# Performance work log

Hardware: AMD Instinct MI355X
Metric: run time of the kernel (lower is better)

## Reference

```python
import jax, jax.numpy as jnp
import numpy as np

MAX_SIZE = 650   # hard-coded node count in the original module
HIDDEN = 512     # hidden_dim
BATCH = 512      # batch_size (conv4 out channels)
IN_DIM = 512
N_EDGES = 150000


def _segment_softmax(e, dst, n):
    # torch_geometric.utils.softmax over destination-node segments
    m = jax.ops.segment_max(e, dst, num_segments=n)
    ex = jnp.exp(e - m[dst])
    s = jax.ops.segment_sum(ex, dst, num_segments=n)
    return ex / (s[dst] + 1e-16)


def _gat_conv(x, src, dst, W, a_src, a_dst, b, n, neg_slope=0.2):
    # PyG GATConv, heads=1, edge_dim=None (edge_attr ignored)
    h = x @ W                            # [n, out]
    al_s = h @ a_src                     # [n] per-node source attention logit
    al_d = h @ a_dst                     # [n] per-node dest attention logit
    e = jax.nn.leaky_relu(al_s[src] + al_d[dst], neg_slope)   # [E]
    alpha = _segment_softmax(e, dst, n)                        # [E]
    out = jax.ops.segment_sum(alpha[:, None] * h[src], dst, num_segments=n)
    return out + b


def setup_inputs() -> dict:
    key = jax.random.key(0)
    ks = jax.random.split(key, 12)
    inp = {
        "x_s": jax.random.normal(ks[0], (400, IN_DIM), jnp.float32),
        "x_t": jax.random.normal(ks[1], (250, IN_DIM), jnp.float32),
        "edge_index": jax.random.randint(ks[2], (2, N_EDGES), 0, MAX_SIZE, dtype=jnp.int32),
        "distances": jax.random.uniform(ks[3], (N_EDGES,), jnp.float32),
        "batch": jnp.zeros((MAX_SIZE,), jnp.int32),
        "W1": jax.random.normal(ks[4], (IN_DIM, HIDDEN), jnp.float32) / np.sqrt(IN_DIM).astype(np.float32),
        "a_src1": jax.random.normal(ks[5], (HIDDEN,), jnp.float32) * 0.1,
        "a_dst1": jax.random.normal(ks[6], (HIDDEN,), jnp.float32) * 0.1,
        "b1": jnp.zeros((HIDDEN,), jnp.float32),
        "W4": jax.random.normal(ks[7], (HIDDEN, BATCH), jnp.float32) / np.sqrt(HIDDEN).astype(np.float32),
        "a_src4": jax.random.normal(ks[8], (BATCH,), jnp.float32) * 0.1,
        "a_dst4": jax.random.normal(ks[9], (BATCH,), jnp.float32) * 0.1,
        "b4": jnp.zeros((BATCH,), jnp.float32),
        "fc_w": jax.random.normal(ks[10], (1, MAX_SIZE), jnp.float32) / np.sqrt(MAX_SIZE).astype(np.float32),
        "fc_b": jnp.zeros((1,), jnp.float32),
    }
    return inp


def reference(x_s, x_t, edge_index, distances, batch,
              W1, a_src1, a_dst1, b1, W4, a_src4, a_dst4, b4, fc_w, fc_b):
    # distances (edge_attr) and batch are unpacked but unused, as in the
    # original (GATConv with edge_dim=None ignores edge_attr).
    x = jnp.concatenate([x_s, x_t], axis=0)
    pad_n = max(MAX_SIZE - x.shape[0], 0)
    x = jnp.pad(x, ((0, pad_n), (0, 0)))            # [650, IN_DIM]
    # add_self_loops=True (PyG GATConv default)
    loop = jnp.arange(MAX_SIZE, dtype=edge_index.dtype)
    src = jnp.concatenate([edge_index[0], loop])
    dst = jnp.concatenate([edge_index[1], loop])
    x = _gat_conv(x, src, dst, W1, a_src1, a_dst1, b1, MAX_SIZE)
    x = jax.nn.relu(x)
    x = _gat_conv(x, src, dst, W4, a_src4, a_dst4, b4, MAX_SIZE)
    x = jax.nn.leaky_relu(x, 0.01)                  # [650, BATCH]
    x = x.reshape(BATCH, MAX_SIZE)                  # torch .view semantics (no transpose)
    x = x @ fc_w.T + fc_b                           # [BATCH, 1]
    x = x.squeeze()[None, :]                        # [1, BATCH]
    return jax.nn.sigmoid(x)
```

## Files before the change

### kernel.cpp

```cpp
#include <hip/hip_runtime.h>
#include <math.h>

#define N_NODES 650
#define DIM     512
#define E_RAW   150000
#define E_TOT   150650
#define WK      672
#define ZG      8
#define ZA      6

__global__ __launch_bounds__(256)
void gemm4(const float* __restrict__ A, const float* __restrict__ Axt,
           const float* __restrict__ B, float* __restrict__ P,
           int M, int lda, int ldb, int kc, int a_mode) {
    __shared__ float Ast[16][68];
    __shared__ float Bs[16][64];
    int t = threadIdx.x;
    int tx4 = (t & 15) * 4, ty4 = (t >> 4) * 4;
    int row0 = blockIdx.y * 64, col0 = blockIdx.x * 64;
    int kbase = blockIdx.z * kc;
    int ar = t >> 2, ak = (t & 3) * 4;
    int bk = t >> 4, bn = (t & 15) * 4;
    float acc[4][4] = {};

    for (int kb = kbase; kb < kbase + kc; kb += 16) {
        {
            int gr = row0 + ar;
            float4 v = make_float4(0.f, 0.f, 0.f, 0.f);
            if (gr < M) {
                const float* rowp;
                if (a_mode == 1)
                    rowp = (gr < 400) ? (A + (size_t)gr * lda) : (Axt + (size_t)(gr - 400) * lda);
                else
                    rowp = A + (size_t)gr * lda;
                v = *(const float4*)(rowp + kb + ak);
            }
            Ast[ak + 0][ar] = v.x; Ast[ak + 1][ar] = v.y;
            Ast[ak + 2][ar] = v.z; Ast[ak + 3][ar] = v.w;
        }
        *(float4*)&Bs[bk][bn] = *(const float4*)&B[(size_t)(kb + bk) * ldb + col0 + bn];
        __syncthreads();
        #pragma unroll
        for (int kk = 0; kk < 16; kk++) {
            float4 a = *(const float4*)&Ast[kk][ty4];
            float4 b = *(const float4*)&Bs[kk][tx4];
            acc[0][0] += a.x*b.x; acc[0][1] += a.x*b.y; acc[0][2] += a.x*b.z; acc[0][3] += a.x*b.w;
            acc[1][0] += a.y*b.x; acc[1][1] += a.y*b.y; acc[1][2] += a.y*b.z; acc[1][3] += a.y*b.w;
            acc[2][0] += a.z*b.x; acc[2][1] += a.z*b.y; acc[2][2] += a.z*b.z; acc[2][3] += a.z*b.w;
            acc[3][0] += a.w*b.x; acc[3][1] += a.w*b.y; acc[3][2] += a.w*b.z; acc[3][3] += a.w*b.w;
        }
        __syncthreads();
    }

    float* Cout = P + (size_t)blockIdx.z * (N_NODES * DIM);
    #pragma unroll
    for (int i = 0; i < 4; i++) {
        int gr = row0 + ty4 + i;
        if (gr < M)
            *(float4*)&Cout[(size_t)gr * DIM + col0 + tx4] =
                make_float4(acc[i][0], acc[i][1], acc[i][2], acc[i][3]);
    }
}

__global__ __launch_bounds__(256)
void reduce_logits(const float* __restrict__ P,
                   const float* __restrict__ asrc, const float* __restrict__ adst,
                   float* __restrict__ h, float* __restrict__ als, float* __restrict__ ald) {
    __shared__ float red[8];
    const size_t S = (size_t)N_NODES * DIM;
    int r = blockIdx.x, t = threadIdx.x;
    size_t base = (size_t)r * DIM;
    float v0 = 0.f, v1 = 0.f;
    #pragma unroll
    for (int z = 0; z < ZG; z++) {
        v0 += P[z * S + base + t];
        v1 += P[z * S + base + t + 256];
    }
    h[base + t]       = v0;
    h[base + t + 256] = v1;
    float ps = v0 * asrc[t] + v1 * asrc[t + 256];
    float pd = v0 * adst[t] + v1 * adst[t + 256];
    #pragma unroll
    for (int o = 32; o > 0; o >>= 1) {
        ps += __shfl_down(ps, o);
        pd += __shfl_down(pd, o);
    }
    if ((t & 63) == 0) { red[t >> 6] = ps; red[4 + (t >> 6)] = pd; }
    __syncthreads();
    if (t == 0) als[r] = red[0] + red[1] + red[2] + red[3];
    if (t == 1) ald[r] = red[4] + red[5] + red[6] + red[7];
}

__global__ __launch_bounds__(256)
void build_w(const int* __restrict__ ei, const float* __restrict__ als,
             const float* __restrict__ ald, float* __restrict__ W,
             float* __restrict__ rs) {
    __shared__ float lrs[N_NODES];
    for (int l = threadIdx.x; l < N_NODES; l += 256) lrs[l] = 0.f;
    __syncthreads();
    int stride = gridDim.x * 256;
    for (int i = blockIdx.x * 256 + threadIdx.x; i < E_TOT; i += stride) {
        int s, d;
        if (i < E_RAW) { s = ei[i]; d = ei[E_RAW + i]; }
        else           { s = d = i - E_RAW; }
        float e = als[s] + ald[d];
        e = e > 0.f ? e : 0.2f * e;
        float ex = __expf(e);
        atomicAdd(&W[(size_t)d * WK + s], ex);
        atomicAdd(&lrs[d], ex);
    }
    __syncthreads();
    for (int l = threadIdx.x; l < N_NODES; l += 256)
        if (lrs[l] != 0.f) atomicAdd(&rs[l], lrs[l]);
}

__global__ __launch_bounds__(256)
void aggred(const float* __restrict__ P, const float* __restrict__ rs,
            const float* __restrict__ bias, float slope, float* __restrict__ o) {
    const size_t S = (size_t)N_NODES * DIM;
    int r = blockIdx.x, t = threadIdx.x;
    size_t base = (size_t)r * DIM;
    float v0 = 0.f, v1 = 0.f;
    #pragma unroll
    for (int z = 0; z < ZA; z++) {
        v0 += P[z * S + base + t];
        v1 += P[z * S + base + t + 256];
    }
    float inv = 1.f / (rs[r] + 1e-16f);
    float a = v0 * inv + bias[t];
    float b = v1 * inv + bias[t + 256];
    o[base + t]       = a > 0.f ? a : slope * a;
    o[base + t + 256] = b > 0.f ? b : slope * b;
}

__global__ void final_kernel(const float* __restrict__ o2,
                             const float* __restrict__ fcw,
                             const float* __restrict__ fcb,
                             float* __restrict__ out) {
    int b = blockIdx.x * 4 + (threadIdx.x >> 6);
    int lane = threadIdx.x & 63;
    if (b >= 512) return;
    float s = 0.f;
    for (int i = lane; i < N_NODES; i += 64)
        s += o2[b * N_NODES + i] * fcw[i];
    #pragma unroll
    for (int o = 32; o > 0; o >>= 1) s += __shfl_down(s, o);
    if (lane == 0) out[b] = 1.f / (1.f + expf(-(s + fcb[0])));
}

extern "C" void kernel_launch(void* const* d_in, const int* in_sizes, int n_in,
                              void* d_out, int out_size, void* d_ws, size_t ws_size,
                              hipStream_t stream) {
    const float* x_s   = (const float*)d_in[0];
    const float* x_t   = (const float*)d_in[1];
    const int*   ei    = (const int*)d_in[2];
    const float* W1    = (const float*)d_in[5];
    const float* asrc1 = (const float*)d_in[6];
    const float* adst1 = (const float*)d_in[7];
    const float* b1    = (const float*)d_in[8];
    const float* W4    = (const float*)d_in[9];
    const float* asrc4 = (const float*)d_in[10];
    const float* adst4 = (const float*)d_in[11];
    const float* b4    = (const float*)d_in[12];
    const float* fcw   = (const float*)d_in[13];
    const float* fcb   = (const float*)d_in[14];
    float* out = (float*)d_out;

    const size_t S = (size_t)N_NODES * DIM;
    float* ws   = (float*)d_ws;
    float* als1 = ws;
    float* ald1 = als1 + N_NODES;
    float* als2 = ald1 + N_NODES;
    float* ald2 = als2 + N_NODES;
    float* P    = ald2 + N_NODES;
    float* o1   = P + (size_t)ZG * S;
    float* o2   = o1 + S;
    float* h    = o2 + S;
    float* W1d  = h + (size_t)WK * DIM;
    float* W2d  = W1d + (size_t)N_NODES * WK;
    float* rs1  = W2d + (size_t)N_NODES * WK;
    float* rs2  = rs1 + N_NODES;

    float* zbeg = h + (size_t)N_NODES * DIM;
    size_t zbytes = (size_t)((WK - N_NODES) * DIM
                           + 2 * N_NODES * WK
                           + 2 * N_NODES) * sizeof(float);
    hipMemsetAsync(zbeg, 0, zbytes, stream);

    dim3 gG(DIM / 64, (N_NODES + 63) / 64, ZG);
    dim3 gA(DIM / 64, (N_NODES + 63) / 64, ZA);

    gemm4<<<gG, 256, 0, stream>>>(x_s, x_t, W1, P, N_NODES, DIM, DIM, 64, 1);
    reduce_logits<<<N_NODES, 256, 0, stream>>>(P, asrc1, adst1, h, als1, ald1);
    build_w<<<128, 256, 0, stream>>>(ei, als1, ald1, W1d, rs1);
    gemm4<<<gA, 256, 0, stream>>>(W1d, nullptr, h, P, N_NODES, WK, DIM, 112, 0);
    aggred<<<N_NODES, 256, 0, stream>>>(P, rs1, b1, 0.0f, o1);

    gemm4<<<gG, 256, 0, stream>>>(o1, nullptr, W4, P, N_NODES, DIM, DIM, 64, 0);
    reduce_logits<<<N_NODES, 256, 0, stream>>>(P, asrc4, adst4, h, als2, ald2);
    build_w<<<128, 256, 0, stream>>>(ei, als2, ald2, W2d, rs2);
    gemm4<<<gA, 256, 0, stream>>>(W2d, nullptr, h, P, N_NODES, WK, DIM, 112, 0);
    aggred<<<N_NODES, 256, 0, stream>>>(P, rs2, b4, 0.01f, o2);

    final_kernel<<<128, 256, 0, stream>>>(o2, fcw, fcb, out);
}
```

Before: 194.7 us.

## Fuse all GAT stages into one cooperative persistent kernel with grid syncs

Replaces the sequence of eleven kernel launches plus a memset with a single cooperative kernel that loops over virtual tiles and rows and separates the stages with grid-wide barriers. Zeroing is done inside the kernel. The aim is to remove per-launch overhead and the idle gaps between the small kernels. The cost is a grid capped at 512 blocks, so the GEMM phases get fewer concurrent blocks than their original tile counts (704 and 528 tiles), and each grid sync adds barrier latency. A non-cooperative fallback path is kept.

```diff
diff --git a/kernel.cpp b/kernel.cpp
--- a/kernel.cpp
+++ b/kernel.cpp
@@ -1,5 +1,8 @@
 #include <hip/hip_runtime.h>
+#include <hip/hip_cooperative_groups.h>
 #include <math.h>
+
+namespace cg = cooperative_groups;
 
 #define N_NODES 650
 #define DIM     512
@@ -8,98 +11,108 @@
 #define WK      672
 #define ZG      8
 #define ZA      6
-
-__global__ __launch_bounds__(256)
-void gemm4(const float* __restrict__ A, const float* __restrict__ Axt,
-           const float* __restrict__ B, float* __restrict__ P,
-           int M, int lda, int ldb, int kc, int a_mode) {
-    __shared__ float Ast[16][68];
-    __shared__ float Bs[16][64];
+#define TILES_X 8
+#define TILES_Y 11
+
+__device__ __forceinline__
+void gemm_phase(const float* __restrict__ A, const float* __restrict__ Axt,
+                const float* __restrict__ B, float* __restrict__ P,
+                int lda, int ldb, int kc, int nvirt, int a_mode, int G,
+                float (* __restrict__ Ast)[68], float (* __restrict__ Bs)[64]) {
     int t = threadIdx.x;
     int tx4 = (t & 15) * 4, ty4 = (t >> 4) * 4;
-    int row0 = blockIdx.y * 64, col0 = blockIdx.x * 64;
-    int kbase = blockIdx.z * kc;
     int ar = t >> 2, ak = (t & 3) * 4;
     int bk = t >> 4, bn = (t & 15) * 4;
-    float acc[4][4] = {};
-
-    for (int kb = kbase; kb < kbase + kc; kb += 16) {
-        {
-            int gr = row0 + ar;
-            float4 v = make_float4(0.f, 0.f, 0.f, 0.f);
-            if (gr < M) {
-                const float* rowp;
-                if (a_mode == 1)
-                    rowp = (gr < 400) ? (A + (size_t)gr * lda) : (Axt + (size_t)(gr - 400) * lda);
-                else
-                    rowp = A + (size_t)gr * lda;
-                v = *(const float4*)(rowp + kb + ak);
+
+    for (int vb = blockIdx.x; vb < nvirt; vb += G) {
+        int bx  = vb & (TILES_X - 1);
+        int rem = vb >> 3;
+        int by  = rem % TILES_Y;
+        int bz  = rem / TILES_Y;
+        int row0 = by * 64, col0 = bx * 64, kbase = bz * kc;
+        float acc[4][4] = {};
+
+        for (int kb = kbase; kb < kbase + kc; kb += 16) {
+            {
+                int gr = row0 + ar;
+                float4 v = make_float4(0.f, 0.f, 0.f, 0.f);
+                if (gr < N_NODES) {
+                    const float* rowp;
+                    if (a_mode == 1)
+                        rowp = (gr < 400) ? (A + (size_t)gr * lda) : (Axt + (size_t)(gr - 400) * lda);
+                    else
+                        rowp = A + (size_t)gr * lda;
+                    v = *(const float4*)(rowp + kb + ak);
+                }
+                Ast[ak + 0][ar] = v.x; Ast[ak + 1][ar] = v.y;
+                Ast[ak + 2][ar] = v.z; Ast[ak + 3][ar] = v.w;
             }
-            Ast[ak + 0][ar] = v.x; Ast[ak + 1][ar] = v.y;
-            Ast[ak + 2][ar] = v.z; Ast[ak + 3][ar] = v.w;
-        }
-        *(float4*)&Bs[bk][bn] = *(const float4*)&B[(size_t)(kb + bk) * ldb + col0 + bn];
+            *(float4*)&Bs[bk][bn] = *(const float4*)&B[(size_t)(kb + bk) * ldb + col0 + bn];
+            __syncthreads();
+            #pragma unroll
+            for (int kk = 0; kk < 16; kk++) {
+                float4 a = *(const float4*)&Ast[kk][ty4];
+                float4 b = *(const float4*)&Bs[kk][tx4];
+                acc[0][0] += a.x*b.x; acc[0][1] += a.x*b.y; acc[0][2] += a.x*b.z; acc[0][3] += a.x*b.w;
+                acc[1][0] += a.y*b.x; acc[1][1] += a.y*b.y; acc[1][2] += a.y*b.z; acc[1][3] += a.y*b.w;
+                acc[2][0] += a.z*b.x; acc[2][1] += a.z*b.y; acc[2][2] += a.z*b.z; acc[2][3] += a.z*b.w;
+                acc[3][0] += a.w*b.x; acc[3][1] += a.w*b.y; acc[3][2] += a.w*b.z; acc[3][3] += a.w*b.w;
+            }
+            __syncthreads();
+        }
+
+        float* Cout = P + (size_t)bz * (N_NODES * DIM);
+        #pragma unroll
+        for (int i = 0; i < 4; i++) {
+            int gr = row0 + ty4 + i;
+            if (gr < N_NODES)
+                *(float4*)&Cout[(size_t)gr * DIM + col0 + tx4] =
+                    make_float4(acc[i][0], acc[i][1], acc[i][2], acc[i][3]);
+        }
+    }
+}
+
+__device__ __forceinline__
+void reduce_phase(const float* __restrict__ P,
+                  const float* __restrict__ asrc, const float* __restrict__ adst,
+                  float* __restrict__ h, float* __restrict__ als, float* __restrict__ ald,
+                  int G, float* __restrict__ red) {
+    const size_t S = (size_t)N_NODES * DIM;
+    int t = threadIdx.x;
+    for (int r = blockIdx.x; r < N_NODES; r += G) {
+        size_t base = (size_t)r * DIM;
+        float v0 = 0.f, v1 = 0.f;
+        #pragma unroll
+        for (int z = 0; z < ZG; z++) {
+            v0 += P[z * S + base + t];
+            v1 += P[z * S + base + t + 256];
+        }
+        h[base + t]       = v0;
+        h[base + t + 256] = v1;
+        float ps = v0 * asrc[t] + v1 * asrc[t + 256];
+        float pd = v0 * adst[t] + v1 * adst[t + 256];
+        #pragma unroll
+        for (int o = 32; o > 0; o >>= 1) {
+            ps += __shfl_down(ps, o);
+            pd += __shfl_down(pd, o);
+        }
+        if ((t & 63) == 0) { red[t >> 6] = ps; red[4 + (t >> 6)] = pd; }
         __syncthreads();
-        #pragma unroll
-        for (int kk = 0; kk < 16; kk++) {
-            float4 a = *(const float4*)&Ast[kk][ty4];
-            float4 b = *(const float4*)&Bs[kk][tx4];
-            acc[0][0] += a.x*b.x; acc[0][1] += a.x*b.y; acc[0][2] += a.x*b.z; acc[0][3] += a.x*b.w;
-            acc[1][0] += a.y*b.x; acc[1][1] += a.y*b.y; acc[1][2] += a.y*b.z; acc[1][3] += a.y*b.w;
-            acc[2][0] += a.z*b.x; acc[2][1] += a.z*b.y; acc[2][2] += a.z*b.z; acc[2][3] += a.z*b.w;
-            acc[3][0] += a.w*b.x; acc[3][1] += a.w*b.y; acc[3][2] += a.w*b.z; acc[3][3] += a.w*b.w;
-        }
+        if (t == 0) als[r] = red[0] + red[1] + red[2] + red[3];
+        if (t == 1) ald[r] = red[4] + red[5] + red[6] + red[7];
         __syncthreads();
     }
-
-    float* Cout = P + (size_t)blockIdx.z * (N_NODES * DIM);
-    #pragma unroll
-    for (int i = 0; i < 4; i++) {
-        int gr = row0 + ty4 + i;
-        if (gr < M)
-            *(float4*)&Cout[(size_t)gr * DIM + col0 + tx4] =
-                make_float4(acc[i][0], acc[i][1], acc[i][2], acc[i][3]);
-    }
-}
-
-__global__ __launch_bounds__(256)
-void reduce_logits(const float* __restrict__ P,
-                   const float* __restrict__ asrc, const float* __restrict__ adst,
-                   float* __restrict__ h, float* __restrict__ als, float* __restrict__ ald) {
-    __shared__ float red[8];
-    const size_t S = (size_t)N_NODES * DIM;
-    int r = blockIdx.x, t = threadIdx.x;
-    size_t base = (size_t)r * DIM;
-    float v0 = 0.f, v1 = 0.f;
-    #pragma unroll
-    for (int z = 0; z < ZG; z++) {
-        v0 += P[z * S + base + t];
-        v1 += P[z * S + base + t + 256];
-    }
-    h[base + t]       = v0;
-    h[base + t + 256] = v1;
-    float ps = v0 * asrc[t] + v1 * asrc[t + 256];
-    float pd = v0 * adst[t] + v1 * adst[t + 256];
-    #pragma unroll
-    for (int o = 32; o > 0; o >>= 1) {
-        ps += __shfl_down(ps, o);
-        pd += __shfl_down(pd, o);
-    }
-    if ((t & 63) == 0) { red[t >> 6] = ps; red[4 + (t >> 6)] = pd; }
+}
+
+__device__ __forceinline__
+void build_phase(const int* __restrict__ ei, const float* __restrict__ als,
+                 const float* __restrict__ ald, float* __restrict__ W,
+                 float* __restrict__ rs, int G, float* __restrict__ lrs) {
+    int t = threadIdx.x;
+    for (int l = t; l < N_NODES; l += 256) lrs[l] = 0.f;
     __syncthreads();
-    if (t == 0) als[r] = red[0] + red[1] + red[2] + red[3];
-    if (t == 1) ald[r] = red[4] + red[5] + red[6] + red[7];
-}
-
-__global__ __launch_bounds__(256)
-void build_w(const int* __restrict__ ei, const float* __restrict__ als,
-             const float* __restrict__ ald, float* __restrict__ W,
-             float* __restrict__ rs) {
-    __shared__ float lrs[N_NODES];
-    for (int l = threadIdx.x; l < N_NODES; l += 256) lrs[l] = 0.f;
-    __syncthreads();
-    int stride = gridDim.x * 256;
-    for (int i = blockIdx.x * 256 + threadIdx.x; i < E_TOT; i += stride) {
+    const int stride = G * 256;
+    for (int i = blockIdx.x * 256 + t; i < E_TOT; i += stride) {
         int s, d;
         if (i < E_RAW) { s = ei[i]; d = ei[E_RAW + i]; }
         else           { s = d = i - E_RAW; }
@@ -110,42 +123,165 @@
         atomicAdd(&lrs[d], ex);
     }
     __syncthreads();
-    for (int l = threadIdx.x; l < N_NODES; l += 256)
+    for (int l = t; l < N_NODES; l += 256)
         if (lrs[l] != 0.f) atomicAdd(&rs[l], lrs[l]);
-}
-
-__global__ __launch_bounds__(256)
-void aggred(const float* __restrict__ P, const float* __restrict__ rs,
-            const float* __restrict__ bias, float slope, float* __restrict__ o) {
+    __syncthreads();
+}
+
+__device__ __forceinline__
+void aggred_phase(const float* __restrict__ P, const float* __restrict__ rs,
+                  const float* __restrict__ bias, float slope, float* __restrict__ o, int G) {
     const size_t S = (size_t)N_NODES * DIM;
-    int r = blockIdx.x, t = threadIdx.x;
-    size_t base = (size_t)r * DIM;
-    float v0 = 0.f, v1 = 0.f;
-    #pragma unroll
-    for (int z = 0; z < ZA; z++) {
-        v0 += P[z * S + base + t];
-        v1 += P[z * S + base + t + 256];
-    }
-    float inv = 1.f / (rs[r] + 1e-16f);
-    float a = v0 * inv + bias[t];
-    float b = v1 * inv + bias[t + 256];
-    o[base + t]       = a > 0.f ? a : slope * a;
-    o[base + t + 256] = b > 0.f ? b : slope * b;
-}
-
-__global__ void final_kernel(const float* __restrict__ o2,
-                             const float* __restrict__ fcw,
-                             const float* __restrict__ fcb,
-                             float* __restrict__ out) {
-    int b = blockIdx.x * 4 + (threadIdx.x >> 6);
-    int lane = threadIdx.x & 63;
-    if (b >= 512) return;
-    float s = 0.f;
-    for (int i = lane; i < N_NODES; i += 64)
-        s += o2[b * N_NODES + i] * fcw[i];
-    #pragma unroll
-    for (int o = 32; o > 0; o >>= 1) s += __shfl_down(s, o);
-    if (lane == 0) out[b] = 1.f / (1.f + expf(-(s + fcb[0])));
+    int t = threadIdx.x;
+    for (int r = blockIdx.x; r < N_NODES; r += G) {
+        size_t base = (size_t)r * DIM;
+        float v0 = 0.f, v1 = 0.f;
+        #pragma unroll
+        for (int z = 0; z < ZA; z++) {
+            v0 += P[z * S + base + t];
+            v1 += P[z * S + base + t + 256];
+        }
+        float inv = 1.f / (rs[r] + 1e-16f);
+        float a = v0 * inv + bias[t];
+        float b = v1 * inv + bias[t + 256];
+        o[base + t]       = a > 0.f ? a : slope * a;
+        o[base + t + 256] = b > 0.f ? b : slope * b;
+    }
+}
+
+__device__ __forceinline__
+void final_phase(const float* __restrict__ o2, const float* __restrict__ fcw,
+                 const float* __restrict__ fcb, float* __restrict__ out,
+                 int G, float* __restrict__ red) {
+    int t = threadIdx.x;
+    for (int b = blockIdx.x; b < 512; b += G) {
+        float s = 0.f;
+        for (int i = t; i < N_NODES; i += 256)
+            s += o2[(size_t)b * N_NODES + i] * fcw[i];
+        #pragma unroll
+        for (int o = 32; o > 0; o >>= 1) s += __shfl_down(s, o);
+        if ((t & 63) == 0) red[t >> 6] = s;
+        __syncthreads();
+        if (t == 0) {
+            float v = red[0] + red[1] + red[2] + red[3] + fcb[0];
+            out[b] = 1.f / (1.f + expf(-v));
+        }
+        __syncthreads();
+    }
+}
+
+__device__ __forceinline__
+void zero_phase(float* __restrict__ zbeg, int nz4, int G) {
+    float4* z4 = (float4*)zbeg;
+    int t = threadIdx.x;
+    for (int i = blockIdx.x * 256 + t; i < nz4; i += G * 256)
+        z4[i] = make_float4(0.f, 0.f, 0.f, 0.f);
+}
+
+__global__ __launch_bounds__(256, 2)
+void gat_fused(const float* __restrict__ x_s, const float* __restrict__ x_t,
+               const int* __restrict__ ei,
+               const float* __restrict__ W1, const float* __restrict__ as1,
+               const float* __restrict__ ad1, const float* __restrict__ b1,
+               const float* __restrict__ W4, const float* __restrict__ as4,
+               const float* __restrict__ ad4, const float* __restrict__ b4,
+               const float* __restrict__ fcw, const float* __restrict__ fcb,
+               float* __restrict__ out, float* __restrict__ ws) {
+    __shared__ float Ast[16][68];
+    __shared__ float Bs[16][64];
+    __shared__ float lrs[N_NODES];
+    __shared__ float red[8];
+
+    const size_t S = (size_t)N_NODES * DIM;
+    float* als1 = ws;
+    float* ald1 = als1 + N_NODES;
+    float* als2 = ald1 + N_NODES;
+    float* ald2 = als2 + N_NODES;
+    float* P    = ald2 + N_NODES;
+    float* o1   = P + (size_t)ZG * S;
+    float* o2   = o1 + S;
+    float* h    = o2 + S;
+    float* W1d  = h + (size_t)WK * DIM;
+    float* W2d  = W1d + (size_t)N_NODES * WK;
+    float* rs1  = W2d + (size_t)N_NODES * WK;
+    float* rs2  = rs1 + N_NODES;
+
+    cg::grid_group grid = cg::this_grid();
+    const int G = gridDim.x;
+
+    {
+        const int nz4 = ((WK - N_NODES) * DIM + 2 * N_NODES * WK + 2 * N_NODES) / 4;
+        zero_phase(h + (size_t)N_NODES * DIM, nz4, G);
+    }
+    gemm_phase(x_s, x_t, W1, P, DIM, DIM, 64, TILES_X * TILES_Y * ZG, 1, G, Ast, Bs);
+    grid.sync();
+
+    reduce_phase(P, as1, ad1, h, als1, ald1, G, red);
+    grid.sync();
+
+    build_phase(ei, als1, ald1, W1d, rs1, G, lrs);
+    grid.sync();
+
+    gemm_phase(W1d, nullptr, h, P, WK, DIM, 112, TILES_X * TILES_Y * ZA, 0, G, Ast, Bs);
+    grid.sync();
+
+    aggred_phase(P, rs1, b1, 0.0f, o1, G);
+    grid.sync();
+
+    gemm_phase(o1, nullptr, W4, P, DIM, DIM, 64, TILES_X * TILES_Y * ZG, 0, G, Ast, Bs);
+    grid.sync();
+
+    reduce_phase(P, as4, ad4, h, als2, ald2, G, red);
+    grid.sync();
+
+    build_phase(ei, als2, ald2, W2d, rs2, G, lrs);
+    grid.sync();
+
+    gemm_phase(W2d, nullptr, h, P, WK, DIM, 112, TILES_X * TILES_Y * ZA, 0, G, Ast, Bs);
+    grid.sync();
+
+    aggred_phase(P, rs2, b4, 0.01f, o2, G);
+    grid.sync();
+
+    final_phase(o2, fcw, fcb, out, G, red);
+}
+
+__global__ __launch_bounds__(256)
+void k_gemm(const float* __restrict__ A, const float* __restrict__ Axt,
+            const float* __restrict__ B, float* __restrict__ P,
+            int lda, int ldb, int kc, int nvirt, int a_mode) {
+    __shared__ float Ast[16][68];
+    __shared__ float Bs[16][64];
+    gemm_phase(A, Axt, B, P, lda, ldb, kc, nvirt, a_mode, gridDim.x, Ast, Bs);
+}
+
+__global__ __launch_bounds__(256)
+void k_reduce(const float* __restrict__ P, const float* __restrict__ asrc,
+              const float* __restrict__ adst, float* __restrict__ h,
+              float* __restrict__ als, float* __restrict__ ald) {
+    __shared__ float red[8];
+    reduce_phase(P, asrc, adst, h, als, ald, gridDim.x, red);
+}
+
+__global__ __launch_bounds__(256)
+void k_build(const int* __restrict__ ei, const float* __restrict__ als,
+             const float* __restrict__ ald, float* __restrict__ W,
+             float* __restrict__ rs) {
+    __shared__ float lrs[N_NODES];
+    build_phase(ei, als, ald, W, rs, gridDim.x, lrs);
+}
+
+__global__ __launch_bounds__(256)
+void k_aggred(const float* __restrict__ P, const float* __restrict__ rs,
+              const float* __restrict__ bias, float slope, float* __restrict__ o) {
+    aggred_phase(P, rs, bias, slope, o, gridDim.x);
+}
+
+__global__ __launch_bounds__(256)
+void k_final(const float* __restrict__ o2, const float* __restrict__ fcw,
+             const float* __restrict__ fcb, float* __restrict__ out) {
+    __shared__ float red[8];
+    final_phase(o2, fcw, fcb, out, gridDim.x, red);
 }
 
 extern "C" void kernel_launch(void* const* d_in, const int* in_sizes, int n_in,
@@ -165,9 +301,9 @@
     const float* fcw   = (const float*)d_in[13];
     const float* fcb   = (const float*)d_in[14];
     float* out = (float*)d_out;
+    float* ws  = (float*)d_ws;
 
     const size_t S = (size_t)N_NODES * DIM;
-    float* ws   = (float*)d_ws;
     float* als1 = ws;
     float* ald1 = als1 + N_NODES;
     float* als2 = ald1 + N_NODES;
@@ -181,26 +317,60 @@
     float* rs1  = W2d + (size_t)N_NODES * WK;
     float* rs2  = rs1 + N_NODES;
 
-    float* zbeg = h + (size_t)N_NODES * DIM;
-    size_t zbytes = (size_t)((WK - N_NODES) * DIM
-                           + 2 * N_NODES * WK
-                           + 2 * N_NODES) * sizeof(float);
-    hipMemsetAsync(zbeg, 0, zbytes, stream);
-
-    dim3 gG(DIM / 64, (N_NODES + 63) / 64, ZG);
-    dim3 gA(DIM / 64, (N_NODES + 63) / 64, ZA);
-
-    gemm4<<<gG, 256, 0, stream>>>(x_s, x_t, W1, P, N_NODES, DIM, DIM, 64, 1);
-    reduce_logits<<<N_NODES, 256, 0, stream>>>(P, asrc1, adst1, h, als1, ald1);
-    build_w<<<128, 256, 0, stream>>>(ei, als1, ald1, W1d, rs1);
-    gemm4<<<gA, 256, 0, stream>>>(W1d, nullptr, h, P, N_NODES, WK, DIM, 112, 0);
-    aggred<<<N_NODES, 256, 0, stream>>>(P, rs1, b1, 0.0f, o1);
-
-    gemm4<<<gG, 256, 0, stream>>>(o1, nullptr, W4, P, N_NODES, DIM, DIM, 64, 0);
-    reduce_logits<<<N_NODES, 256, 0, stream>>>(P, asrc4, adst4, h, als2, ald2);
-    build_w<<<128, 256, 0, stream>>>(ei, als2, ald2, W2d, rs2);
-    gemm4<<<gA, 256, 0, stream>>>(W2d, nullptr, h, P, N_NODES, WK, DIM, 112, 0);
-    aggred<<<N_NODES, 256, 0, stream>>>(P, rs2, b4, 0.01f, o2);
-
-    final_kernel<<<128, 256, 0, stream>>>(o2, fcw, fcb, out);
-}
+    static int coop_blocks = -2;
+    if (coop_blocks == -2) {
+        int maxB = 0;
+        hipError_t e = hipOccupancyMaxActiveBlocksPerMultiprocessor(
+            &maxB, (const void*)gat_fused, 256, 0);
+        if (e == hipSuccess && maxB >= 1) {
+            hipDeviceProp_t prop;
+            int dev = 0;
+            hipGetDevice(&dev);
+            if (hipGetDeviceProperties(&prop, dev) == hipSuccess && prop.multiProcessorCount > 0) {
+                long cap = (long)maxB * prop.multiProcessorCount;
+                coop_blocks = (int)(cap < 512 ? cap : 512);
+            } else {
+                coop_blocks = -1;
+            }
+        } else {
+            coop_blocks = -1;
+        }
+    }
+
+    bool done = false;
+    if (coop_blocks > 0) {
+        void* args[] = {
+            (void*)&x_s, (void*)&x_t, (void*)&ei,
+            (void*)&W1, (void*)&asrc1, (void*)&adst1, (void*)&b1,
+            (void*)&W4, (void*)&asrc4, (void*)&adst4, (void*)&b4,
+            (void*)&fcw, (void*)&fcb, (void*)&out, (void*)&ws
+        };
+        hipError_t e = hipLaunchCooperativeKernel((const void*)gat_fused,
+                                                  dim3(coop_blocks), dim3(256),
+                                                  args, 0, stream);
+        if (e == hipSuccess) done = true;
+        else coop_blocks = -1;
+    }
+
+    if (!done) {
+        float* zbeg = h + (size_t)N_NODES * DIM;
+        size_t zbytes = (size_t)((WK - N_NODES) * DIM
+                               + 2 * N_NODES * WK
+                               + 2 * N_NODES) * sizeof(float);
+        hipMemsetAsync(zbeg, 0, zbytes, stream);
+
+        k_gemm<<<512, 256, 0, stream>>>(x_s, x_t, W1, P, DIM, DIM, 64, TILES_X * TILES_Y * ZG, 1);
+        k_reduce<<<N_NODES, 256, 0, stream>>>(P, asrc1, adst1, h, als1, ald1);
+        k_build<<<128, 256, 0, stream>>>(ei, als1, ald1, W1d, rs1);
+        k_gemm<<<512, 256, 0, stream>>>(W1d, nullptr, h, P, WK, DIM, 112, TILES_X * TILES_Y * ZA, 0);
+        k_aggred<<<N_NODES, 256, 0, stream>>>(P, rs1, b1, 0.0f, o1);
+
+        k_gemm<<<512, 256, 0, stream>>>(o1, nullptr, W4, P, DIM, DIM, 64, TILES_X * TILES_Y * ZG, 0);
+        k_reduce<<<N_NODES, 256, 0, stream>>>(P, asrc4, adst4, h, als2, ald2);
+        k_build<<<128, 256, 0, stream>>>(ei, als2, ald2, W2d, rs2);
+        k_gemm<<<512, 256, 0, stream>>>(W2d, nullptr, h, P, WK, DIM, 112, TILES_X * TILES_Y * ZA, 0);
+        k_aggred<<<N_NODES, 256, 0, stream>>>(P, rs2, b4, 0.01f, o2);
+
+        k_final<<<512, 256, 0, stream>>>(o2, fcw, fcb, out);
+    }
+}
```

Result: slower. 525.0 us (+169.7%).

## Fuse split-K reductions into GEMM epilogues and drop partial-sum buffers

Applied to the files above, without the earlier changes.

Removes split-K from both GEMM stages. Attention logits are computed in the feature GEMM epilogue via shuffles and atomics, and normalization, bias and activation are applied in the aggregation GEMM epilogue. This eliminates the separate reduce kernels and the large partial-sum buffer traffic. In exchange, each GEMM launches far fewer blocks with a much longer K loop, which reduces parallelism across CUs.

```diff
diff --git a/kernel.cpp b/kernel.cpp
--- a/kernel.cpp
+++ b/kernel.cpp
@@ -6,39 +6,36 @@
 #define E_RAW   150000
 #define E_TOT   150650
 #define WK      672
-#define ZG      8
-#define ZA      6
 
 __global__ __launch_bounds__(256)
-void gemm4(const float* __restrict__ A, const float* __restrict__ Axt,
-           const float* __restrict__ B, float* __restrict__ P,
-           int M, int lda, int ldb, int kc, int a_mode) {
+void k_feat(const float* __restrict__ A, const float* __restrict__ Axt,
+            const float* __restrict__ B,
+            const float* __restrict__ asrc, const float* __restrict__ adst,
+            float* __restrict__ h, float* __restrict__ als, float* __restrict__ ald,
+            int a_mode) {
     __shared__ float Ast[16][68];
     __shared__ float Bs[16][64];
     int t = threadIdx.x;
     int tx4 = (t & 15) * 4, ty4 = (t >> 4) * 4;
     int row0 = blockIdx.y * 64, col0 = blockIdx.x * 64;
-    int kbase = blockIdx.z * kc;
     int ar = t >> 2, ak = (t & 3) * 4;
     int bk = t >> 4, bn = (t & 15) * 4;
     float acc[4][4] = {};
 
-    for (int kb = kbase; kb < kbase + kc; kb += 16) {
+    for (int kb = 0; kb < DIM; kb += 16) {
         {
             int gr = row0 + ar;
             float4 v = make_float4(0.f, 0.f, 0.f, 0.f);
-            if (gr < M) {
-                const float* rowp;
-                if (a_mode == 1)
-                    rowp = (gr < 400) ? (A + (size_t)gr * lda) : (Axt + (size_t)(gr - 400) * lda);
-                else
-                    rowp = A + (size_t)gr * lda;
+            if (gr < N_NODES) {
+                const float* rowp = (a_mode == 1)
+                    ? ((gr < 400) ? A + (size_t)gr * DIM : Axt + (size_t)(gr - 400) * DIM)
+                    : A + (size_t)gr * DIM;
                 v = *(const float4*)(rowp + kb + ak);
             }
             Ast[ak + 0][ar] = v.x; Ast[ak + 1][ar] = v.y;
             Ast[ak + 2][ar] = v.z; Ast[ak + 3][ar] = v.w;
         }
-        *(float4*)&Bs[bk][bn] = *(const float4*)&B[(size_t)(kb + bk) * ldb + col0 + bn];
+        *(float4*)&Bs[bk][bn] = *(const float4*)&B[(size_t)(kb + bk) * DIM + col0 + bn];
         __syncthreads();
         #pragma unroll
         for (int kk = 0; kk < 16; kk++) {
@@ -52,54 +49,39 @@
         __syncthreads();
     }
 
-    float* Cout = P + (size_t)blockIdx.z * (N_NODES * DIM);
+    float4 as4 = *(const float4*)&asrc[col0 + tx4];
+    float4 ad4 = *(const float4*)&adst[col0 + tx4];
     #pragma unroll
     for (int i = 0; i < 4; i++) {
         int gr = row0 + ty4 + i;
-        if (gr < M)
-            *(float4*)&Cout[(size_t)gr * DIM + col0 + tx4] =
+        float sa = acc[i][0]*as4.x + acc[i][1]*as4.y + acc[i][2]*as4.z + acc[i][3]*as4.w;
+        float sd = acc[i][0]*ad4.x + acc[i][1]*ad4.y + acc[i][2]*ad4.z + acc[i][3]*ad4.w;
+        #pragma unroll
+        for (int o = 8; o > 0; o >>= 1) {
+            sa += __shfl_down(sa, o, 16);
+            sd += __shfl_down(sd, o, 16);
+        }
+        if (gr < N_NODES) {
+            *(float4*)&h[(size_t)gr * DIM + col0 + tx4] =
                 make_float4(acc[i][0], acc[i][1], acc[i][2], acc[i][3]);
+            if ((t & 15) == 0) {
+                atomicAdd(&als[gr], sa);
+                atomicAdd(&ald[gr], sd);
+            }
+        }
     }
 }
 
 __global__ __launch_bounds__(256)
-void reduce_logits(const float* __restrict__ P,
-                   const float* __restrict__ asrc, const float* __restrict__ adst,
-                   float* __restrict__ h, float* __restrict__ als, float* __restrict__ ald) {
-    __shared__ float red[8];
-    const size_t S = (size_t)N_NODES * DIM;
-    int r = blockIdx.x, t = threadIdx.x;
-    size_t base = (size_t)r * DIM;
-    float v0 = 0.f, v1 = 0.f;
-    #pragma unroll
-    for (int z = 0; z < ZG; z++) {
-        v0 += P[z * S + base + t];
-        v1 += P[z * S + base + t + 256];
-    }
-    h[base + t]       = v0;
-    h[base + t + 256] = v1;
-    float ps = v0 * asrc[t] + v1 * asrc[t + 256];
-    float pd = v0 * adst[t] + v1 * adst[t + 256];
-    #pragma unroll
-    for (int o = 32; o > 0; o >>= 1) {
-        ps += __shfl_down(ps, o);
-        pd += __shfl_down(pd, o);
-    }
-    if ((t & 63) == 0) { red[t >> 6] = ps; red[4 + (t >> 6)] = pd; }
-    __syncthreads();
-    if (t == 0) als[r] = red[0] + red[1] + red[2] + red[3];
-    if (t == 1) ald[r] = red[4] + red[5] + red[6] + red[7];
-}
-
-__global__ __launch_bounds__(256)
-void build_w(const int* __restrict__ ei, const float* __restrict__ als,
+void k_build(const int* __restrict__ ei, const float* __restrict__ als,
              const float* __restrict__ ald, float* __restrict__ W,
              float* __restrict__ rs) {
     __shared__ float lrs[N_NODES];
-    for (int l = threadIdx.x; l < N_NODES; l += 256) lrs[l] = 0.f;
+    int t = threadIdx.x;
+    for (int l = t; l < N_NODES; l += 256) lrs[l] = 0.f;
     __syncthreads();
-    int stride = gridDim.x * 256;
-    for (int i = blockIdx.x * 256 + threadIdx.x; i < E_TOT; i += stride) {
+    const int stride = gridDim.x * 256;
+    for (int i = blockIdx.x * 256 + t; i < E_TOT; i += stride) {
         int s, d;
         if (i < E_RAW) { s = ei[i]; d = ei[E_RAW + i]; }
         else           { s = d = i - E_RAW; }
@@ -110,39 +92,75 @@
         atomicAdd(&lrs[d], ex);
     }
     __syncthreads();
-    for (int l = threadIdx.x; l < N_NODES; l += 256)
+    for (int l = t; l < N_NODES; l += 256)
         if (lrs[l] != 0.f) atomicAdd(&rs[l], lrs[l]);
 }
 
 __global__ __launch_bounds__(256)
-void aggred(const float* __restrict__ P, const float* __restrict__ rs,
-            const float* __restrict__ bias, float slope, float* __restrict__ o) {
-    const size_t S = (size_t)N_NODES * DIM;
-    int r = blockIdx.x, t = threadIdx.x;
-    size_t base = (size_t)r * DIM;
-    float v0 = 0.f, v1 = 0.f;
+void k_agg(const float* __restrict__ W, const float* __restrict__ Bm,
+           const float* __restrict__ rs, const float* __restrict__ bias,
+           float slope, float* __restrict__ o) {
+    __shared__ float Ast[16][68];
+    __shared__ float Bs[16][64];
+    int t = threadIdx.x;
+    int tx4 = (t & 15) * 4, ty4 = (t >> 4) * 4;
+    int row0 = blockIdx.y * 64, col0 = blockIdx.x * 64;
+    int ar = t >> 2, ak = (t & 3) * 4;
+    int bk = t >> 4, bn = (t & 15) * 4;
+    float acc[4][4] = {};
+
+    for (int kb = 0; kb < WK; kb += 16) {
+        {
+            int gr = row0 + ar;
+            float4 v = make_float4(0.f, 0.f, 0.f, 0.f);
+            if (gr < N_NODES)
+                v = *(const float4*)(W + (size_t)gr * WK + kb + ak);
+            Ast[ak + 0][ar] = v.x; Ast[ak + 1][ar] = v.y;
+            Ast[ak + 2][ar] = v.z; Ast[ak + 3][ar] = v.w;
+        }
+        *(float4*)&Bs[bk][bn] = *(const float4*)&Bm[(size_t)(kb + bk) * DIM + col0 + bn];
+        __syncthreads();
+        #pragma unroll
+        for (int kk = 0; kk < 16; kk++) {
+            float4 a = *(const float4*)&Ast[kk][ty4];
+            float4 b = *(const float4*)&Bs[kk][tx4];
+            acc[0][0] += a.x*b.x; acc[0][1] += a.x*b.y; acc[0][2] += a.x*b.z; acc[0][3] += a.x*b.w;
+            acc[1][0] += a.y*b.x; acc[1][1] += a.y*b.y; acc[1][2] += a.y*b.z; acc[1][3] += a.y*b.w;
+            acc[2][0] += a.z*b.x; acc[2][1] += a.z*b.y; acc[2][2] += a.z*b.z; acc[2][3] += a.z*b.w;
+            acc[3][0] += a.w*b.x; acc[3][1] += a.w*b.y; acc[3][2] += a.w*b.z; acc[3][3] += a.w*b.w;
+        }
+        __syncthreads();
+    }
+
+    float4 bb = *(const float4*)&bias[col0 + tx4];
     #pragma unroll
-    for (int z = 0; z < ZA; z++) {
-        v0 += P[z * S + base + t];
-        v1 += P[z * S + base + t + 256];
-    }
-    float inv = 1.f / (rs[r] + 1e-16f);
-    float a = v0 * inv + bias[t];
-    float b = v1 * inv + bias[t + 256];
-    o[base + t]       = a > 0.f ? a : slope * a;
-    o[base + t + 256] = b > 0.f ? b : slope * b;
-}
-
-__global__ void final_kernel(const float* __restrict__ o2,
-                             const float* __restrict__ fcw,
-                             const float* __restrict__ fcb,
-                             float* __restrict__ out) {
+    for (int i = 0; i < 4; i++) {
+        int gr = row0 + ty4 + i;
+        if (gr < N_NODES) {
+            float inv = 1.f / (rs[gr] + 1e-16f);
+            float v0 = acc[i][0] * inv + bb.x;
+            float v1 = acc[i][1] * inv + bb.y;
+            float v2 = acc[i][2] * inv + bb.z;
+            float v3 = acc[i][3] * inv + bb.w;
+            v0 = v0 > 0.f ? v0 : slope * v0;
+            v1 = v1 > 0.f ? v1 : slope * v1;
+            v2 = v2 > 0.f ? v2 : slope * v2;
+            v3 = v3 > 0.f ? v3 : slope * v3;
+            *(float4*)&o[(size_t)gr * DIM + col0 + tx4] = make_float4(v0, v1, v2, v3);
+        }
+    }
+}
+
+__global__ void k_final(const float* __restrict__ o2,
+                        const float* __restrict__ fcw,
+                        const float* __restrict__ fcb,
+                        float* __restrict__ out) {
     int b = blockIdx.x * 4 + (threadIdx.x >> 6);
     int lane = threadIdx.x & 63;
     if (b >= 512) return;
     float s = 0.f;
     for (int i = lane; i < N_NODES; i += 64)
-        s += o2[b * N_NODES + i] * fcw[i];
+        s += o2[(size_t)b * N_NODES + i] * fcw[i];
     #pragma unroll
     for (int o = 32; o > 0; o >>= 1) s += __shfl_down(s, o);
     if (lane == 0) out[b] = 1.f / (1.f + expf(-(s + fcb[0])));
@@ -166,41 +184,35 @@
     const float* fcb   = (const float*)d_in[14];
     float* out = (float*)d_out;
 
-    const size_t S = (size_t)N_NODES * DIM;
     float* ws   = (float*)d_ws;
-    float* als1 = ws;
+    float* h    = ws;
+    float* als1 = h + (size_t)WK * DIM;
     float* ald1 = als1 + N_NODES;
     float* als2 = ald1 + N_NODES;
     float* ald2 = als2 + N_NODES;
-    float* P    = ald2 + N_NODES;
-    float* o1   = P + (size_t)ZG * S;
-    float* o2   = o1 + S;
-    float* h    = o2 + S;
-    float* W1d  = h + (size_t)WK * DIM;
+    float* rs1  = ald2 + N_NODES;
+    float* rs2  = rs1 + N_NODES;
+    float* W1d  = rs2 + N_NODES;
     float* W2d  = W1d + (size_t)N_NODES * WK;
-    float* rs1  = W2d + (size_t)N_NODES * WK;
-    float* rs2  = rs1 + N_NODES;
+    float* o1   = W2d + (size_t)N_NODES * WK;
+    float* o2   = o1 + (size_t)N_NODES * DIM;
 
     float* zbeg = h + (size_t)N_NODES * DIM;
     size_t zbytes = (size_t)((WK - N_NODES) * DIM
-                           + 2 * N_NODES * WK
-                           + 2 * N_NODES) * sizeof(float);
+                           + 6 * N_NODES
+                           + 2 * N_NODES * WK)
+                    * sizeof(float);
     hipMemsetAsync(zbeg, 0, zbytes, stream);
 
-    dim3 gG(DIM / 64, (N_NODES + 63) / 64, ZG);
-    dim3 gA(DIM / 64, (N_NODES + 63) / 64, ZA);
-
-    gemm4<<<gG, 256, 0, stream>>>(x_s, x_t, W1, P, N_NODES, DIM, DIM, 64, 1);
-    reduce_logits<<<N_NODES, 256, 0, stream>>>(P, asrc1, adst1, h, als1, ald1);
-    build_w<<<128, 256, 0, stream>>>(ei, als1, ald1, W1d, rs1);
-    gemm4<<<gA, 256, 0, stream>>>(W1d, nullptr, h, P, N_NODES, WK, DIM, 112, 0);
-    aggred<<<N_NODES, 256, 0, stream>>>(P, rs1, b1, 0.0f, o1);
-
-    gemm4<<<gG, 256, 0, stream>>>(o1, nullptr, W4, P, N_NODES, DIM, DIM, 64, 0);
-    reduce_logits<<<N_NODES, 256, 0, stream>>>(P, asrc4, adst4, h, als2, ald2);
-    build_w<<<128, 256, 0, stream>>>(ei, als2, ald2, W2d, rs2);
-    gemm4<<<gA, 256, 0, stream>>>(W2d, nullptr, h, P, N_NODES, WK, DIM, 112, 0);
-    aggred<<<N_NODES, 256, 0, stream>>>(P, rs2, b4, 0.01f, o2);
-
-    final_kernel<<<128, 256, 0, stream>>>(o2, fcw, fcb, out);
-}
+    dim3 gT(DIM / 64, (N_NODES + 63) / 64);
+
+    k_feat<<<gT, 256, 0, stream>>>(x_s, x_t, W1, asrc1, adst1, h, als1, ald1, 1);
+    k_build<<<128, 256, 0, stream>>>(ei, als1, ald1, W1d, rs1);
+    k_agg<<<gT, 256, 0, stream>>>(W1d, h, rs1, b1, 0.0f, o1);
+
+    k_feat<<<gT, 256, 0, stream>>>(o1, nullptr, W4, asrc4, adst4, h, als2, ald2, 0);
+    k_build<<<128, 256, 0, stream>>>(ei, als2, ald2, W2d, rs2);
+    k_agg<<<gT, 256, 0, stream>>>(W2d, h, rs2, b4, 0.01f, o2);
+
+    k_final<<<128, 256, 0, stream>>>(o2, fcw, fcb, out);
+}
```

Result: slower. 255.6 us (+31.3%).
